# Optimization experiments

Hardware: AMD Instinct MI355X
Metric: run time of the kernel (lower is better)

## Reference

```python
import jax, jax.numpy as jnp
import numpy as np

DIM = 256
EPS = 1e-8


def rmsnorm(y, scale):
    # full RMSNorm (p < 0): rms = ||y||_2 / sqrt(d)
    norm = jnp.linalg.norm(y, axis=-1, keepdims=True)
    rms = norm * (DIM ** -0.5)
    return scale * (y / (rms + EPS))


def setup_inputs() -> dict:
    key = jax.random.key(0)
    ks = jax.random.split(key, 12)
    d = DIM
    inp = {
        "agent": jax.random.normal(ks[0], (64, d), dtype=jnp.float32),
        "x": jax.random.normal(ks[1], (8, 8192, d), dtype=jnp.float32),
        "W_qkv": jax.random.normal(ks[2], (3 * d, d), dtype=jnp.float32) * 0.02,
        "b_qkv": jnp.zeros((3 * d,), dtype=jnp.float32),
        "W_agent": jax.random.normal(ks[3], (2 * d, d), dtype=jnp.float32) * 0.02,
        "b_agent": jnp.zeros((2 * d,), dtype=jnp.float32),
        "W_fc1": jax.random.normal(ks[4], (d, d), dtype=jnp.float32) * 0.02,
        "b_fc1": jnp.zeros((d,), dtype=jnp.float32),
        "W_fc2": jax.random.normal(ks[5], (d, d), dtype=jnp.float32) * 0.02,
        "b_fc2": jnp.zeros((d,), dtype=jnp.float32),
        "norm_scale": jnp.ones((d,), dtype=jnp.float32),
    }
    return inp


def reference(agent, x, W_qkv, b_qkv, W_agent, b_agent, W_fc1, b_fc1, W_fc2, b_fc2, norm_scale):
    sc = DIM ** -0.5
    # qkv projection of x: [B, N, 3d] -> q, k, v each [B, N, d]
    qkv = x @ W_qkv.T + b_qkv
    q, k, v = jnp.split(qkv, 3, axis=-1)
    # agent projection: [K, 2d] -> q_agent, k_agent each [K, d]
    qa_ka = agent @ W_agent.T + b_agent
    q_agent, k_agent = jnp.split(qa_ka, 2, axis=-1)
    # stage 1: agents attend over tokens  -> [B, K, N]
    attn1 = jax.nn.softmax(jnp.einsum('kd,bnd->bkn', q_agent, k) * sc, axis=-1)
    v1 = jnp.einsum('bkn,bnd->bkd', attn1, v)  # [B, K, d]
    v1 = v1 @ W_fc1.T + b_fc1
    # stage 2: tokens attend over agents -> [B, N, K]
    attn2 = jax.nn.softmax(jnp.einsum('bnd,kd->bnk', q, k_agent) * sc, axis=-1)
    v2 = jnp.einsum('bnk,bkd->bnd', attn2, v1)  # [B, N, d]
    v2 = v2 @ W_fc2.T + b_fc2
    return rmsnorm(v2 + x, norm_scale)
```

## Files before the change

kernel.cpp:

```cpp
#include <hip/hip_runtime.h>
#include <hip/hip_bf16.h>

typedef __attribute__((ext_vector_type(4))) float f32x4;
typedef __attribute__((ext_vector_type(8))) short s16x8;
typedef __attribute__((ext_vector_type(4))) short s16x4;

__device__ __forceinline__ unsigned short f2bf(float f) {
    unsigned int u; __builtin_memcpy(&u, &f, 4);
    u += 0x7fffu + ((u >> 16) & 1u);
    return (unsigned short)(u >> 16);
}
__device__ __forceinline__ float bf2f(unsigned short h) {
    unsigned int u = ((unsigned int)h) << 16;
    float f; __builtin_memcpy(&f, &u, 4);
    return f;
}
__device__ __forceinline__ s16x8 pack8(f32x4 a, f32x4 b) {
    s16x8 r;
    r[0] = (short)f2bf(a[0]); r[1] = (short)f2bf(a[1]);
    r[2] = (short)f2bf(a[2]); r[3] = (short)f2bf(a[3]);
    r[4] = (short)f2bf(b[0]); r[5] = (short)f2bf(b[1]);
    r[6] = (short)f2bf(b[2]); r[7] = (short)f2bf(b[3]);
    return r;
}

__global__ __launch_bounds__(256) void build_M2(
    const float* __restrict__ W_qkv, const float* __restrict__ b_qkv,
    const float* __restrict__ agent, const float* __restrict__ W_agent,
    const float* __restrict__ b_agent,
    const float* __restrict__ W_fc1, const float* __restrict__ W_fc2,
    unsigned short* __restrict__ MS, float* __restrict__ cbias,
    unsigned short* __restrict__ Wb)
{
    const int i = blockIdx.x;
    const int t = threadIdx.x;
    if (i >= 128) {
        const int R0 = (i - 128) * 4;
        #pragma unroll
        for (int rr = 0; rr < 4; ++rr) {
            const int R = R0 + rr;
            const float* src = (R < 256) ? W_qkv + (size_t)(512 + R) * 256
                             : (R < 512) ? W_fc1 + (size_t)(R - 256) * 256
                                         : W_fc2 + (size_t)(R - 512) * 256;
            Wb[(size_t)R * 256 + t] = f2bf(src[t]);
        }
        return;
    }
    __shared__ float ag[256];
    __shared__ float qs[256];
    const int a = i & 63;
    const bool isS1 = (i < 64);
    ag[t] = agent[(size_t)a * 256 + t];
    __syncthreads();
    const int tp = isS1 ? t : 256 + t;
    {
        const float* wr = W_agent + (size_t)tp * 256;
        float q = 0.f;
        #pragma unroll 4
        for (int d = 0; d < 256; d += 4) {
            f32x4 wv = *(const f32x4*)(wr + d);
            q += ag[d] * wv[0] + ag[d + 1] * wv[1] + ag[d + 2] * wv[2] + ag[d + 3] * wv[3];
        }
        qs[t] = (q + b_agent[tp]) * 0.0625f;
    }
    __syncthreads();
    const float* W  = W_qkv + (isS1 ? 256 * 256 : 0);
    const float* bb = b_qkv + (isS1 ? 256 : 0);
    float acc = 0.f, cb = 0.f;
    for (int dout = 0; dout < 256; ++dout) {
        const float q = qs[dout];
        acc += q * W[(size_t)dout * 256 + t];
        cb  += q * bb[dout];
    }
    MS[i * 256 + t] = f2bf(acc);
    if (t == 0) cbias[i] = cb;
}

__global__ __launch_bounds__(256) void xproj2(
    const float* __restrict__ x,
    const unsigned short* __restrict__ MS,
    const float* __restrict__ cbias,
    float* __restrict__ S1T,
    unsigned short* __restrict__ P2,
    float* __restrict__ mpart, float* __restrict__ lpart)
{
    __shared__ alignas(16) unsigned short As[64 * 256];
    const int tid = threadIdx.x, lane = tid & 63, w = tid >> 6;
    const int lr = lane & 15, lq = lane >> 4;
    const long m0 = (long)blockIdx.x * 64;

    {
        const int k0 = (tid & 31) * 8;
        #pragma unroll
        for (int j = 0; j < 8; ++j) {
            const int row = (tid >> 5) + j * 8;
            const float* s = x + (m0 + row) * 256 + k0;
            f32x4 f0 = *(const f32x4*)s;
            f32x4 f1 = *(const f32x4*)(s + 4);
            *(s16x8*)((char*)As + row * 512 + ((k0 * 2) ^ ((row & 7) << 4))) = pack8(f0, f1);
        }
    }
    __syncthreads();

    f32x4 acc[4][2];
    const f32x4 zero = {0.f, 0.f, 0.f, 0.f};
    #pragma unroll
    for (int rf = 0; rf < 4; ++rf)
        #pragma unroll
        for (int j = 0; j < 2; ++j)
            acc[rf][j] = zero;

    #pragma unroll
    for (int ks = 0; ks < 8; ++ks) {
        const int kb = ks * 64 + lq * 16;
        s16x8 areg[4];
        #pragma unroll
        for (int rf = 0; rf < 4; ++rf) {
            const int row = rf * 16 + lr;
            areg[rf] = *(const s16x8*)((const char*)As + row * 512 + (kb ^ ((row & 7) << 4)));
        }
        s16x8 bfr[2];
        #pragma unroll
        for (int j = 0; j < 2; ++j) {
            const int msrow = j * 64 + w * 16 + lr;
            bfr[j] = *(const s16x8*)((const char*)MS + (size_t)msrow * 512 + kb);
        }
        #pragma unroll
        for (int rf = 0; rf < 4; ++rf)
            #pragma unroll
            for (int j = 0; j < 2; ++j)
                acc[rf][j] = __builtin_amdgcn_mfma_f32_16x16x32_bf16(
                    areg[rf], bfr[j], acc[rf][j], 0, 0, 0);
    }

    {
        const int a = w * 16 + lr;
        const float bv = cbias[a];
        float mx = -1e30f;
        #pragma unroll
        for (int rf = 0; rf < 4; ++rf)
            #pragma unroll
            for (int r = 0; r < 4; ++r) {
                const float v = acc[rf][0][r] + bv;
                S1T[(m0 + rf * 16 + lq * 4 + r) * 64 + a] = v;
                mx = fmaxf(mx, v);
            }
        mx = fmaxf(mx, __shfl_xor(mx, 16));
        mx = fmaxf(mx, __shfl_xor(mx, 32));
        float sm = 0.f;
        #pragma unroll
        for (int rf = 0; rf < 4; ++rf)
            #pragma unroll
            for (int r = 0; r < 4; ++r)
                sm += __expf(acc[rf][0][r] + bv - mx);
        sm += __shfl_xor(sm, 16);
        sm += __shfl_xor(sm, 32);
        if (lq == 0) {
            mpart[(size_t)blockIdx.x * 64 + a] = mx;
            lpart[(size_t)blockIdx.x * 64 + a] = sm;
        }
    }

    __syncthreads();
    {
        float* SC = (float*)As;
        const int a = w * 16 + lr;
        const float bv = cbias[64 + a];
        #pragma unroll
        for (int rf = 0; rf < 4; ++rf)
            #pragma unroll
            for (int r = 0; r < 4; ++r) {
                const int n = rf * 16 + lq * 4 + r;
                SC[n * 68 + a] = acc[rf][1][r] + bv;
            }
    }
    __syncthreads();
    {
        const float* SC = (const float*)As;
        const int t4 = lane >> 2, q = lane & 3;
        const int nl = w * 16 + t4;
        f32x4 sv[4];
        #pragma unroll
        for (int j = 0; j < 4; ++j) sv[j] = *(const f32x4*)&SC[nl * 68 + q * 16 + j * 4];
        float mx = -1e30f;
        #pragma unroll
        for (int j = 0; j < 4; ++j)
            #pragma unroll
            for (int e = 0; e < 4; ++e) mx = fmaxf(mx, sv[j][e]);
        mx = fmaxf(mx, __shfl_xor(mx, 1));
        mx = fmaxf(mx, __shfl_xor(mx, 2));
        float p[16];
        float sm = 0.f;
        #pragma unroll
        for (int j = 0; j < 4; ++j)
            #pragma unroll
            for (int e = 0; e < 4; ++e) {
                p[j * 4 + e] = __expf(sv[j][e] - mx);
                sm += p[j * 4 + e];
            }
        sm += __shfl_xor(sm, 1);
        sm += __shfl_xor(sm, 2);
        const float rs = 1.f / sm;
        s16x8 o0, o1;
        #pragma unroll
        for (int e = 0; e < 8; ++e) o0[e] = (short)f2bf(p[e] * rs);
        #pragma unroll
        for (int e = 0; e < 8; ++e) o1[e] = (short)f2bf(p[8 + e] * rs);
        const int swz = (nl & 7) << 4;
        char* row = (char*)P2 + (m0 + nl) * 128;
        *(s16x8*)(row + ((q * 32) ^ swz)) = o0;
        *(s16x8*)(row + ((q * 32 + 16) ^ swz)) = o1;
    }
}

__global__ __launch_bounds__(256) void pv_mfma2(
    const float* __restrict__ S1T,
    const float* __restrict__ x,
    const float* __restrict__ mpart,
    const float* __restrict__ lpart,
    float* __restrict__ y_part)
{
    __shared__ alignas(16) unsigned short P_lds[64 * 128];
    __shared__ alignas(16) unsigned short XT[128 * 136];
    const int tid = threadIdx.x, lane = tid & 63, w = tid >> 6;
    const int lr = lane & 15, lq = lane >> 4;
    const int c = blockIdx.x, dh = blockIdx.y, b = blockIdx.z;
    const int a4 = (tid & 15) * 4;

    f32x4 m4, l4;
    {
        float* scratch = (float*)XT;
        const int a = tid & 63, s4 = tid >> 6;
        const size_t bb = (size_t)b * 128;
        float M = -1e30f;
        for (int cc = s4; cc < 128; cc += 4)
            M = fmaxf(M, mpart[(bb + cc) * 64 + a]);
        float L = 0.f;
        for (int cc = s4; cc < 128; cc += 4) {
            const size_t idx = (bb + cc) * 64 + a;
            L += lpart[idx] * __expf(mpart[idx] - M);
        }
        scratch[tid] = M;
        scratch[256 + tid] = L;
        __syncthreads();
        if (tid < 64) {
            float Mm = scratch[tid];
            #pragma unroll
            for (int ss = 1; ss < 4; ++ss) Mm = fmaxf(Mm, scratch[ss * 64 + tid]);
            float Ll = 0.f;
            #pragma unroll
            for (int ss = 0; ss < 4; ++ss)
                Ll += scratch[256 + ss * 64 + tid] * __expf(scratch[ss * 64 + tid] - Mm);
            scratch[512 + tid] = Mm;
            scratch[576 + tid] = 1.0f / Ll;
        }
        __syncthreads();
        #pragma unroll
        for (int j = 0; j < 4; ++j) {
            m4[j] = scratch[512 + a4 + j];
            l4[j] = scratch[576 + a4 + j];
        }
        __syncthreads();
    }

    f32x4 acc[4][2];
    const f32x4 zero = {0.f, 0.f, 0.f, 0.f};
    #pragma unroll
    for (int rf = 0; rf < 4; ++rf)
        #pragma unroll
        for (int cf = 0; cf < 2; ++cf)
            acc[rf][cf] = zero;

    for (int kt = 0; kt < 2; ++kt) {
        const size_t ng0 = (size_t)b * 8192 + c * 256 + kt * 128;
        #pragma unroll
        for (int pass = 0; pass < 4; ++pass) {
            const int np = 2 * (tid >> 4) + pass * 32;
            const float* s = S1T + (ng0 + np) * 64 + a4;
            f32x4 s0 = *(const f32x4*)s;
            f32x4 s1 = *(const f32x4*)(s + 64);
            #pragma unroll
            for (int j = 0; j < 4; ++j) {
                const int a = a4 + j;
                const float p0 = __expf(s0[j] - m4[j]) * l4[j];
                const float p1 = __expf(s1[j] - m4[j]) * l4[j];
                const unsigned int pk = (unsigned int)f2bf(p0) | ((unsigned int)f2bf(p1) << 16);
                *(unsigned int*)((char*)P_lds + a * 256 + ((np * 2) ^ (((a >> 1) & 7) << 4))) = pk;
            }
        }
        {
            const int nh = tid >> 2;
            const int dq = tid & 3;
            const float* xbase = x + (ng0 + 2 * nh) * 256 + dh * 128;
            #pragma unroll
            for (int pass = 0; pass < 8; ++pass) {
                const int dl0 = pass * 16 + dq * 4;
                f32x4 xa = *(const f32x4*)(xbase + dl0);
                f32x4 xb = *(const f32x4*)(xbase + 256 + dl0);
                #pragma unroll
                for (int jj = 0; jj < 4; ++jj) {
                    const unsigned int pk = (unsigned int)f2bf(xa[jj]) | ((unsigned int)f2bf(xb[jj]) << 16);
                    *(unsigned int*)((char*)XT + (dl0 + jj) * 272 + nh * 4) = pk;
                }
            }
        }
        __syncthreads();
        #pragma unroll
        for (int ks = 0; ks < 4; ++ks) {
            const int kbn = ks * 64 + lq * 16;
            s16x8 af[4], bfv[2];
            #pragma unroll
            for (int rf = 0; rf < 4; ++rf) {
                const int row = rf * 16 + lr;
                af[rf] = *(const s16x8*)((const char*)P_lds + row * 256 + (kbn ^ (((row >> 1) & 7) << 4)));
            }
            #pragma unroll
            for (int cf = 0; cf < 2; ++cf) {
                const int dl = w * 32 + cf * 16 + lr;
                bfv[cf] = *(const s16x8*)((const char*)XT + dl * 272 + kbn);
            }
            #pragma unroll
            for (int rf = 0; rf < 4; ++rf)
                #pragma unroll
                for (int cf = 0; cf < 2; ++cf)
                    acc[rf][cf] = __builtin_amdgcn_mfma_f32_16x16x32_bf16(
                        af[rf], bfv[cf], acc[rf][cf], 0, 0, 0);
        }
        __syncthreads();
    }
    #pragma unroll
    for (int rf = 0; rf < 4; ++rf)
        #pragma unroll
        for (int cf = 0; cf < 2; ++cf)
            #pragma unroll
            for (int r = 0; r < 4; ++r) {
                const int a = rf * 16 + lq * 4 + r;
                const int d = dh * 128 + w * 32 + cf * 16 + lr;
                y_part[(((size_t)b * 32 + c) * 64 + a) * 256 + d] = acc[rf][cf][r];
            }
}

__global__ __launch_bounds__(256) void chain_fused(
    const float* __restrict__ y_part,
    const unsigned short* __restrict__ Wb,
    const float* __restrict__ b_qkv,
    const float* __restrict__ b_fc1,
    const float* __restrict__ b_fc2,
    float* __restrict__ uu)
{
    __shared__ alignas(16) unsigned short A0[16 * 256];
    __shared__ alignas(16) unsigned short A1[16 * 256];
    const int tid = threadIdx.x, lane = tid & 63, w = tid >> 6;
    const int lr = lane & 15, lq = lane >> 4;
    const int rg = blockIdx.x, b = blockIdx.y;
    const int a0 = rg * 16;

    {
        const int d0 = lane * 4;
        f32x4 r4[4];
        const f32x4 zero = {0.f, 0.f, 0.f, 0.f};
        #pragma unroll
        for (int j = 0; j < 4; ++j) r4[j] = zero;
        for (int c = 0; c < 32; ++c) {
            const float* base = y_part + (((size_t)b * 32 + c) * 64 + a0 + w * 4) * 256 + d0;
            #pragma unroll
            for (int j = 0; j < 4; ++j)
                r4[j] += *(const f32x4*)(base + (size_t)j * 256);
        }
        #pragma unroll
        for (int j = 0; j < 4; ++j) {
            const int a = w * 4 + j;
            s16x4 pk;
            #pragma unroll
            for (int e = 0; e < 4; ++e) pk[e] = (short)f2bf(r4[j][e]);
            *(s16x4*)((char*)A0 + a * 512 + ((d0 * 2) ^ ((a & 7) << 4))) = pk;
        }
    }
    __syncthreads();

    unsigned short* bufA = A0;
    unsigned short* bufB = A1;
    for (int s = 0; s < 3; ++s) {
        const unsigned short* W = Wb + (size_t)s * 65536;
        const float* bias = (s == 0) ? (b_qkv + 512) : (s == 1) ? b_fc1 : b_fc2;
        f32x4 acc[4];
        const f32x4 zero = {0.f, 0.f, 0.f, 0.f};
        #pragma unroll
        for (int cf = 0; cf < 4; ++cf) acc[cf] = zero;
        #pragma unroll
        for (int ks = 0; ks < 8; ++ks) {
            const int kb = ks * 64 + lq * 16;
            const int row = lr;
            s16x8 af = *(const s16x8*)((const char*)bufA + row * 512 + (kb ^ ((row & 7) << 4)));
            s16x8 bf[4];
            #pragma unroll
            for (int cf = 0; cf < 4; ++cf) {
                const int col = w * 64 + cf * 16 + lr;
                bf[cf] = *(const s16x8*)((const char*)W + (size_t)col * 512 + kb);
            }
            #pragma unroll
            for (int cf = 0; cf < 4; ++cf)
                acc[cf] = __builtin_amdgcn_mfma_f32_16x16x32_bf16(af, bf[cf], acc[cf], 0, 0, 0);
        }
        if (s < 2) {
            #pragma unroll
            for (int cf = 0; cf < 4; ++cf) {
                const int col = w * 64 + cf * 16 + lr;
                const float bv = bias[col];
                #pragma unroll
                for (int r = 0; r < 4; ++r) {
                    const int a = lq * 4 + r;
                    *(unsigned short*)((char*)bufB + a * 512 + ((col * 2) ^ ((a & 7) << 4)))
                        = f2bf(acc[cf][r] + bv);
                }
            }
            __syncthreads();
            unsigned short* t = bufA; bufA = bufB; bufB = t;
        } else {
            #pragma unroll
            for (int cf = 0; cf < 4; ++cf) {
                const int col = w * 64 + cf * 16 + lr;
                const float bv = bias[col];
                #pragma unroll
                for (int r = 0; r < 4; ++r) {
                    const int a = a0 + lq * 4 + r;
                    uu[((size_t)b * 64 + a) * 256 + col] = acc[cf][r] + bv;
                }
            }
        }
    }
}

__global__ __launch_bounds__(256) void stage2_final(const unsigned short* __restrict__ P2,
                                                    const float* __restrict__ uu,
                                                    const float* __restrict__ x,
                                                    const float* __restrict__ nscale,
                                                    float* __restrict__ out)
{
    __shared__ alignas(16) unsigned short uT[256 * 64];
    __shared__ alignas(16) unsigned short P[64 * 64];
    __shared__ float ssq[4][64];
    const int tid = threadIdx.x, lane = tid & 63, w = tid >> 6;
    const int lr = lane & 15, lq = lane >> 4;
    const int b = blockIdx.x >> 7;
    const long n0 = (long)blockIdx.x * 64;

    {
        const int pr = tid >> 3;
        const int sub = tid & 7;
        const float* u0 = uu + ((size_t)b * 64 + 2 * pr) * 256;
        #pragma unroll
        for (int pass = 0; pass < 8; ++pass) {
            const int d0 = pass * 32 + sub * 4;
            f32x4 ua = *(const f32x4*)(u0 + d0);
            f32x4 ub = *(const f32x4*)(u0 + 256 + d0);
            #pragma unroll
            for (int jj = 0; jj < 4; ++jj) {
                const int d = d0 + jj;
                const unsigned int pk = (unsigned int)f2bf(ua[jj]) | ((unsigned int)f2bf(ub[jj]) << 16);
                *(unsigned int*)((char*)uT + d * 128 + ((pr * 4) ^ ((d & 7) << 4))) = pk;
            }
        }
    }
    {
        const int row = tid & 63, seg = tid >> 6;
        const char* src = (const char*)P2 + (n0 + row) * 128 + seg * 32;
        s16x8 v0 = *(const s16x8*)src;
        s16x8 v1 = *(const s16x8*)(src + 16);
        *(s16x8*)((char*)P + row * 128 + seg * 32) = v0;
        *(s16x8*)((char*)P + row * 128 + seg * 32 + 16) = v1;
    }
    __syncthreads();

    f32x4 acc[4][4];
    const f32x4 zero = {0.f, 0.f, 0.f, 0.f};
    #pragma unroll
    for (int rf = 0; rf < 4; ++rf)
        #pragma unroll
        for (int cf = 0; cf < 4; ++cf)
            acc[rf][cf] = zero;
    #pragma unroll
    for (int ks = 0; ks < 2; ++ks) {
        const int kb = ks * 64 + lq * 16;
        s16x8 af[4], bfv[4];
        #pragma unroll
        for (int rf = 0; rf < 4; ++rf) {
            const int dR = w * 64 + rf * 16 + lr;
            af[rf] = *(const s16x8*)((const char*)uT + dR * 128 + (kb ^ ((dR & 7) << 4)));
        }
        #pragma unroll
        for (int cf = 0; cf < 4; ++cf) {
            const int nR = cf * 16 + lr;
            bfv[cf] = *(const s16x8*)((const char*)P + nR * 128 + (kb ^ ((nR & 7) << 4)));
        }
        #pragma unroll
        for (int rf = 0; rf < 4; ++rf)
            #pragma unroll
            for (int cf = 0; cf < 4; ++cf)
                acc[rf][cf] = __builtin_amdgcn_mfma_f32_16x16x32_bf16(
                    af[rf], bfv[cf], acc[rf][cf], 0, 0, 0);
    }

    float part[4] = {0.f, 0.f, 0.f, 0.f};
    #pragma unroll
    for (int cf = 0; cf < 4; ++cf) {
        const long n = n0 + cf * 16 + lr;
        #pragma unroll
        for (int rf = 0; rf < 4; ++rf) {
            const int d0 = w * 64 + rf * 16 + lq * 4;
            const f32x4 xr = *(const f32x4*)&x[n * 256 + d0];
            acc[rf][cf] += xr;
            part[cf] += acc[rf][cf][0] * acc[rf][cf][0] + acc[rf][cf][1] * acc[rf][cf][1]
                      + acc[rf][cf][2] * acc[rf][cf][2] + acc[rf][cf][3] * acc[rf][cf][3];
        }
    }
    #pragma unroll
    for (int cf = 0; cf < 4; ++cf) {
        float s = part[cf];
        s += __shfl_xor(s, 16);
        s += __shfl_xor(s, 32);
        if (lq == 0) ssq[w][cf * 16 + lr] = s;
    }
    __syncthreads();

    #pragma unroll
    for (int cf = 0; cf < 4; ++cf) {
        const int tokl = cf * 16 + lr;
        const float tot = ssq[0][tokl] + ssq[1][tokl] + ssq[2][tokl] + ssq[3][tokl];
        const float inv = 1.f / (sqrtf(tot) * 0.0625f + 1e-8f);
        const long n = n0 + tokl;
        #pragma unroll
        for (int rf = 0; rf < 4; ++rf) {
            const int d0 = w * 64 + rf * 16 + lq * 4;
            const f32x4 sc4 = *(const f32x4*)&nscale[d0];
            f32x4 o = sc4 * acc[rf][cf] * inv;
            *(f32x4*)&out[n * 256 + d0] = o;
        }
    }
}

extern "C" void kernel_launch(void* const* d_in, const int* in_sizes, int n_in,
                              void* d_out, int out_size, void* d_ws, size_t ws_size,
                              hipStream_t stream)
{
    const float* agent   = (const float*)d_in[0];
    const float* x       = (const float*)d_in[1];
    const float* W_qkv   = (const float*)d_in[2];
    const float* b_qkv   = (const float*)d_in[3];
    const float* W_agent = (const float*)d_in[4];
    const float* b_agent = (const float*)d_in[5];
    const float* W_fc1   = (const float*)d_in[6];
    const float* b_fc1   = (const float*)d_in[7];
    const float* W_fc2   = (const float*)d_in[8];
    const float* b_fc2   = (const float*)d_in[9];
    const float* nscale  = (const float*)d_in[10];
    float* out = (float*)d_out;

    char* wsp = (char*)d_ws;
    size_t off = 0;
    auto alloc = [&](size_t n) { void* p = wsp + off; off += (n + 255) & ~(size_t)255; return p; };

    unsigned short* MS = (unsigned short*)alloc(128UL * 256 * 2);
    float*  cbias  = (float*)alloc(128UL * 4);
    unsigned short* Wb = (unsigned short*)alloc(3UL * 256 * 256 * 2);
    float*  S1T    = (float*)alloc(65536UL * 64 * 4);
    unsigned short* P2 = (unsigned short*)alloc(65536UL * 64 * 2);
    float*  mpart  = (float*)alloc(1024UL * 64 * 4);
    float*  lpart  = (float*)alloc(1024UL * 64 * 4);
    float*  y_part = (float*)alloc(8UL * 32 * 64 * 256 * 4);
    float*  uu     = (float*)alloc(512UL * 256 * 4);

    build_M2<<<320, 256, 0, stream>>>(W_qkv, b_qkv, agent, W_agent, b_agent,
                                      W_fc1, W_fc2, MS, cbias, Wb);
    xproj2<<<1024, 256, 0, stream>>>(x, MS, cbias, S1T, P2, mpart, lpart);
    pv_mfma2<<<dim3(32, 2, 8), 256, 0, stream>>>(S1T, x, mpart, lpart, y_part);
    chain_fused<<<dim3(4, 8), 256, 0, stream>>>(y_part, Wb, b_qkv, b_fc1, b_fc2, uu);
    stage2_final<<<1024, 256, 0, stream>>>(P2, uu, x, nscale, out);
}
```

Baseline: 121.1 us.

## Store intermediates in bf16 with pre-exponentiated stage-1 scores and pre-transposed agent values

```diff
diff --git a/kernel.cpp b/kernel.cpp
--- a/kernel.cpp
+++ b/kernel.cpp
@@ -80,7 +80,7 @@
     const float* __restrict__ x,
     const unsigned short* __restrict__ MS,
     const float* __restrict__ cbias,
-    float* __restrict__ S1T,
+    unsigned short* __restrict__ S1b,
     unsigned short* __restrict__ P2,
     float* __restrict__ mpart, float* __restrict__ lpart)
 {
@@ -136,14 +136,14 @@
     {
         const int a = w * 16 + lr;
         const float bv = cbias[a];
+        float vv[4][4];
         float mx = -1e30f;
         #pragma unroll
         for (int rf = 0; rf < 4; ++rf)
             #pragma unroll
             for (int r = 0; r < 4; ++r) {
-                const float v = acc[rf][0][r] + bv;
-                S1T[(m0 + rf * 16 + lq * 4 + r) * 64 + a] = v;
-                mx = fmaxf(mx, v);
+                vv[rf][r] = acc[rf][0][r] + bv;
+                mx = fmaxf(mx, vv[rf][r]);
             }
         mx = fmaxf(mx, __shfl_xor(mx, 16));
         mx = fmaxf(mx, __shfl_xor(mx, 32));
@@ -151,8 +151,11 @@
         #pragma unroll
         for (int rf = 0; rf < 4; ++rf)
             #pragma unroll
-            for (int r = 0; r < 4; ++r)
-                sm += __expf(acc[rf][0][r] + bv - mx);
+            for (int r = 0; r < 4; ++r) {
+                const float p = __expf(vv[rf][r] - mx);
+                sm += p;
+                S1b[(m0 + rf * 16 + lq * 4 + r) * 64 + a] = f2bf(p);
+            }
         sm += __shfl_xor(sm, 16);
         sm += __shfl_xor(sm, 32);
         if (lq == 0) {
@@ -214,11 +217,11 @@
 }
 
 __global__ __launch_bounds__(256) void pv_mfma2(
-    const float* __restrict__ S1T,
+    const unsigned short* __restrict__ S1b,
     const float* __restrict__ x,
     const float* __restrict__ mpart,
     const float* __restrict__ lpart,
-    float* __restrict__ y_part)
+    unsigned short* __restrict__ y_partb)
 {
     __shared__ alignas(16) unsigned short P_lds[64 * 128];
     __shared__ alignas(16) unsigned short XT[128 * 136];
@@ -273,17 +276,25 @@
 
     for (int kt = 0; kt < 2; ++kt) {
         const size_t ng0 = (size_t)b * 8192 + c * 256 + kt * 128;
+        const size_t lc0 = (size_t)b * 128 + c * 4 + kt * 2;
+        f32x4 corr0, corr1;
+        #pragma unroll
+        for (int j = 0; j < 4; ++j) {
+            corr0[j] = __expf(mpart[lc0 * 64 + a4 + j] - m4[j]) * l4[j];
+            corr1[j] = __expf(mpart[(lc0 + 1) * 64 + a4 + j] - m4[j]) * l4[j];
+        }
         #pragma unroll
         for (int pass = 0; pass < 4; ++pass) {
             const int np = 2 * (tid >> 4) + pass * 32;
-            const float* s = S1T + (ng0 + np) * 64 + a4;
-            f32x4 s0 = *(const f32x4*)s;
-            f32x4 s1 = *(const f32x4*)(s + 64);
+            const unsigned short* s = S1b + (ng0 + np) * 64 + a4;
+            s16x4 r0 = *(const s16x4*)s;
+            s16x4 r1 = *(const s16x4*)(s + 64);
+            const f32x4 corr = (pass < 2) ? corr0 : corr1;
             #pragma unroll
             for (int j = 0; j < 4; ++j) {
                 const int a = a4 + j;
-                const float p0 = __expf(s0[j] - m4[j]) * l4[j];
-                const float p1 = __expf(s1[j] - m4[j]) * l4[j];
+                const float p0 = bf2f((unsigned short)r0[j]) * corr[j];
+                const float p1 = bf2f((unsigned short)r1[j]) * corr[j];
                 const unsigned int pk = (unsigned int)f2bf(p0) | ((unsigned int)f2bf(p1) << 16);
                 *(unsigned int*)((char*)P_lds + a * 256 + ((np * 2) ^ (((a >> 1) & 7) << 4))) = pk;
             }
@@ -336,17 +347,17 @@
             for (int r = 0; r < 4; ++r) {
                 const int a = rf * 16 + lq * 4 + r;
                 const int d = dh * 128 + w * 32 + cf * 16 + lr;
-                y_part[(((size_t)b * 32 + c) * 64 + a) * 256 + d] = acc[rf][cf][r];
+                y_partb[(((size_t)b * 32 + c) * 64 + a) * 256 + d] = f2bf(acc[rf][cf][r]);
             }
 }
 
 __global__ __launch_bounds__(256) void chain_fused(
-    const float* __restrict__ y_part,
+    const unsigned short* __restrict__ y_partb,
     const unsigned short* __restrict__ Wb,
     const float* __restrict__ b_qkv,
     const float* __restrict__ b_fc1,
     const float* __restrict__ b_fc2,
-    float* __restrict__ uu)
+    unsigned short* __restrict__ uTg)
 {
     __shared__ alignas(16) unsigned short A0[16 * 256];
     __shared__ alignas(16) unsigned short A1[16 * 256];
@@ -362,10 +373,15 @@
         #pragma unroll
         for (int j = 0; j < 4; ++j) r4[j] = zero;
         for (int c = 0; c < 32; ++c) {
-            const float* base = y_part + (((size_t)b * 32 + c) * 64 + a0 + w * 4) * 256 + d0;
-            #pragma unroll
-            for (int j = 0; j < 4; ++j)
-                r4[j] += *(const f32x4*)(base + (size_t)j * 256);
+            const unsigned short* base = y_partb + (((size_t)b * 32 + c) * 64 + a0 + w * 4) * 256 + d0;
+            #pragma unroll
+            for (int j = 0; j < 4; ++j) {
+                s16x4 v = *(const s16x4*)(base + (size_t)j * 256);
+                r4[j][0] += bf2f((unsigned short)v[0]);
+                r4[j][1] += bf2f((unsigned short)v[1]);
+                r4[j][2] += bf2f((unsigned short)v[2]);
+                r4[j][3] += bf2f((unsigned short)v[3]);
+            }
         }
         #pragma unroll
         for (int j = 0; j < 4; ++j) {
@@ -424,7 +440,7 @@
                 #pragma unroll
                 for (int r = 0; r < 4; ++r) {
                     const int a = a0 + lq * 4 + r;
-                    uu[((size_t)b * 64 + a) * 256 + col] = acc[cf][r] + bv;
+                    uTg[((size_t)b * 256 + col) * 64 + a] = f2bf(acc[cf][r] + bv);
                 }
             }
         }
@@ -432,7 +448,7 @@
 }
 
 __global__ __launch_bounds__(256) void stage2_final(const unsigned short* __restrict__ P2,
-                                                    const float* __restrict__ uu,
+                                                    const unsigned short* __restrict__ uTg,
                                                     const float* __restrict__ x,
                                                     const float* __restrict__ nscale,
                                                     float* __restrict__ out)
@@ -446,20 +462,12 @@
     const long n0 = (long)blockIdx.x * 64;
 
     {
-        const int pr = tid >> 3;
-        const int sub = tid & 7;
-        const float* u0 = uu + ((size_t)b * 64 + 2 * pr) * 256;
-        #pragma unroll
-        for (int pass = 0; pass < 8; ++pass) {
-            const int d0 = pass * 32 + sub * 4;
-            f32x4 ua = *(const f32x4*)(u0 + d0);
-            f32x4 ub = *(const f32x4*)(u0 + 256 + d0);
-            #pragma unroll
-            for (int jj = 0; jj < 4; ++jj) {
-                const int d = d0 + jj;
-                const unsigned int pk = (unsigned int)f2bf(ua[jj]) | ((unsigned int)f2bf(ub[jj]) << 16);
-                *(unsigned int*)((char*)uT + d * 128 + ((pr * 4) ^ ((d & 7) << 4))) = pk;
-            }
+        const char* src = (const char*)uTg + (size_t)b * 256 * 128 + tid * 128;
+        const int swz = (tid & 7) << 4;
+        #pragma unroll
+        for (int seg = 0; seg < 8; ++seg) {
+            s16x8 v = *(const s16x8*)(src + seg * 16);
+            *(s16x8*)((char*)uT + tid * 128 + ((seg * 16) ^ swz)) = v;
         }
     }
     {
@@ -563,17 +571,17 @@
     unsigned short* MS = (unsigned short*)alloc(128UL * 256 * 2);
     float*  cbias  = (float*)alloc(128UL * 4);
     unsigned short* Wb = (unsigned short*)alloc(3UL * 256 * 256 * 2);
-    float*  S1T    = (float*)alloc(65536UL * 64 * 4);
-    unsigned short* P2 = (unsigned short*)alloc(65536UL * 64 * 2);
+    unsigned short* S1b = (unsigned short*)alloc(65536UL * 64 * 2);
+    unsigned short* P2  = (unsigned short*)alloc(65536UL * 64 * 2);
     float*  mpart  = (float*)alloc(1024UL * 64 * 4);
     float*  lpart  = (float*)alloc(1024UL * 64 * 4);
-    float*  y_part = (float*)alloc(8UL * 32 * 64 * 256 * 4);
-    float*  uu     = (float*)alloc(512UL * 256 * 4);
+    unsigned short* y_partb = (unsigned short*)alloc(8UL * 32 * 64 * 256 * 2);
+    unsigned short* uTg = (unsigned short*)alloc(8UL * 256 * 64 * 2);
 
     build_M2<<<320, 256, 0, stream>>>(W_qkv, b_qkv, agent, W_agent, b_agent,
                                       W_fc1, W_fc2, MS, cbias, Wb);
-    xproj2<<<1024, 256, 0, stream>>>(x, MS, cbias, S1T, P2, mpart, lpart);
-    pv_mfma2<<<dim3(32, 2, 8), 256, 0, stream>>>(S1T, x, mpart, lpart, y_part);
-    chain_fused<<<dim3(4, 8), 256, 0, stream>>>(y_part, Wb, b_qkv, b_fc1, b_fc2, uu);
-    stage2_final<<<1024, 256, 0, stream>>>(P2, uu, x, nscale, out);
-}
+    xproj2<<<1024, 256, 0, stream>>>(x, MS, cbias, S1b, P2, mpart, lpart);
+    pv_mfma2<<<dim3(32, 2, 8), 256, 0, stream>>>(S1b, x, mpart, lpart, y_partb);
+    chain_fused<<<dim3(4, 8), 256, 0, stream>>>(y_partb, Wb, b_qkv, b_fc1, b_fc2, uTg);
+    stage2_final<<<1024, 256, 0, stream>>>(P2, uTg, x, nscale, out);
+}
```

Result: slower. 127.8 us (+5.5%).
